# Kernel optimization log

Hardware: AMD Instinct MI355X
Metric: run time of the kernel (lower is better)

Reference implementation:

```python
import jax, jax.numpy as jnp
import numpy as np

NEG = -1e30  # stand-in for -inf on the H-attention diagonal (matches INF helper)


def _conv1x1(w, b, x):
    # w: [O, C], x: [B, C, H, W]
    return jnp.einsum('oc,bchw->bohw', w, x) + b[None, :, None, None]


def _cc_attn(q, k, v):
    """Criss-cross attention: q,k [B,Cq,H,W], v [B,C,H,W] -> [B,C,H,W]."""
    B, _, H, W = q.shape
    # column (H) energies: query at (h,w) attends to keys at (h', w)
    eH = jnp.einsum('bchw,bcjw->bhwj', q, k)  # [B,H,W,H]
    eye = jnp.eye(H, dtype=bool)[None, :, None, :]
    eH = jnp.where(eye, NEG, eH)  # mask h==h' (self counted once via W pass)
    # row (W) energies: query at (h,w) attends to keys at (h, w')
    eW = jnp.einsum('bchw,bchj->bhwj', q, k)  # [B,H,W,W]
    att = jax.nn.softmax(jnp.concatenate([eH, eW], axis=3), axis=3)  # [B,H,W,H+W]
    aH, aW = att[..., :H], att[..., H:]
    outH = jnp.einsum('bhwj,bcjw->bchw', aH, v)
    outW = jnp.einsum('bhwj,bchj->bchw', aW, v)
    return outH + outW


def setup_inputs() -> dict:
    key = jax.random.key(0)
    ks = jax.random.split(key, 14)
    B, C, H, W = 8, 256, 96, 96
    Cq = C // 8
    n = jax.random.normal
    return {
        'x': n(ks[0], (B, C, H, W), jnp.float32),
        'y': n(ks[1], (B, C, H, W), jnp.float32),
        'Wq': n(ks[2], (Cq, C), jnp.float32) * 0.05,
        'bq': n(ks[3], (Cq,), jnp.float32) * 0.05,
        'Wk': n(ks[4], (Cq, C), jnp.float32) * 0.05,
        'bk': n(ks[5], (Cq,), jnp.float32) * 0.05,
        'Wv': n(ks[6], (C, C), jnp.float32) * 0.05,
        'bv': n(ks[7], (C,), jnp.float32) * 0.05,
        'gamma1': n(ks[8], (1,), jnp.float32) * 0.1,
        'gamma2': n(ks[9], (1,), jnp.float32) * 0.1,
        'Wd': n(ks[10], (2 * C, 1, 3, 3), jnp.float32) * 0.1,  # depthwise, groups=2C
        'bd': n(ks[11], (2 * C,), jnp.float32) * 0.05,
        'Wp': n(ks[12], (C, 2 * C), jnp.float32) * 0.05,  # pointwise 1x1
        'bp': n(ks[13], (C,), jnp.float32) * 0.05,
    }


def reference(x, y, Wq, bq, Wk, bk, Wv, bv, gamma1, gamma2, Wd, bd, Wp, bp):
    qx = _conv1x1(Wq, bq, x)
    kx = _conv1x1(Wk, bk, x)
    vx = _conv1x1(Wv, bv, x)
    qy = _conv1x1(Wq, bq, y)
    ky = _conv1x1(Wk, bk, y)
    vy = _conv1x1(Wv, bv, y)
    # pass 1: attention weights from x, values from y
    out1 = gamma1[0] * _cc_attn(qx, kx, vy) + x
    # pass 2: attention weights from y, values from x
    out2 = gamma2[0] * _cc_attn(qy, ky, vx) + y
    z = jnp.concatenate([out1, out2], axis=1)  # [B, 2C, H, W]
    # depthwise 3x3 (groups = 2C), padding 1
    z = jax.lax.conv_general_dilated(
        z, Wd, window_strides=(1, 1), padding='SAME',
        feature_group_count=z.shape[1],
        dimension_numbers=('NCHW', 'OIHW', 'NCHW')) + bd[None, :, None, None]
    # pointwise 1x1 then LeakyReLU (torch default negative_slope=0.01)
    z = _conv1x1(Wp, bp, z)
    return jax.nn.leaky_relu(z, negative_slope=0.01)
```

## Files before the change

kernel.cpp:

```cpp
#include <hip/hip_runtime.h>
#include <hip/hip_bf16.h>

constexpr int kB  = 8;
constexpr int kC  = 256;
constexpr int kCq = 32;
constexpr int kH  = 96;
constexpr int kW  = 96;
constexpr int kP  = kH * kW;

using bf16x8 = __attribute__((ext_vector_type(8))) short;
using bf16x4 = __attribute__((ext_vector_type(4))) short;
using f32x4  = __attribute__((ext_vector_type(4))) float;

__device__ inline bf16x8 ld_lds8(const __hip_bfloat16* p) {
    bf16x4 lo = *(const bf16x4*)p;
    bf16x4 hi = *(const bf16x4*)(p + 4);
    return __builtin_shufflevector(lo, hi, 0, 1, 2, 3, 4, 5, 6, 7);
}

__global__ __launch_bounds__(256) void w_convert(
    const float* __restrict__ Wq, const float* __restrict__ Wk,
    const float* __restrict__ Wv,
    __hip_bfloat16* __restrict__ Wqkb, __hip_bfloat16* __restrict__ Wvb)
{
    const int i = blockIdx.x * 256 + threadIdx.x;
    if (i < 8192)       Wqkb[i] = __float2bfloat16(Wq[i]);
    else if (i < 16384) Wqkb[i] = __float2bfloat16(Wk[i - 8192]);
    else                Wvb[i - 16384] = __float2bfloat16(Wv[i - 16384]);
}

__global__ __launch_bounds__(256, 2) void qkv_mfma(
    const float* __restrict__ in_qk, const float* __restrict__ in_v,
    const __hip_bfloat16* __restrict__ Wqkb, const __hip_bfloat16* __restrict__ Wvb,
    const float* __restrict__ bq, const float* __restrict__ bk,
    const float* __restrict__ bv,
    __hip_bfloat16* __restrict__ Qbh, __hip_bfloat16* __restrict__ Qbl,
    __hip_bfloat16* __restrict__ Kbh, __hip_bfloat16* __restrict__ Kbl,
    __hip_bfloat16* __restrict__ Vpm, __hip_bfloat16* __restrict__ Vhw)
{
    __shared__ __align__(16) char smem[34816];
    __hip_bfloat16* sqb = (__hip_bfloat16*)smem;
    __hip_bfloat16* svb = sqb + 2 * 64 * 36;
    __hip_bfloat16* vt  = (__hip_bfloat16*)smem;

    const int b = blockIdx.y, t = threadIdx.x;
    const int wv = t >> 6, l = t & 63;
    const int n = l & 15, q = l >> 4;
    const int p0 = blockIdx.x * 64;
    const int p  = p0 + wv * 16 + n;
    const size_t bP = (size_t)b * kP;

    const float* __restrict__ xq = in_qk + (size_t)b * kC * kP + p0;
    const float* __restrict__ xv = in_v  + (size_t)b * kC * kP + p0;

    const int sc = t >> 4;
    const int sp = (t & 15) * 4;

    f32x4 acc[20];
#pragma unroll
    for (int i = 0; i < 20; i++) acc[i] = (f32x4)0.f;

    {
        float4 q0 = *(const float4*)&xq[(size_t)sc * kP + sp];
        float4 q1 = *(const float4*)&xq[(size_t)(16 + sc) * kP + sp];
        float4 v0 = *(const float4*)&xv[(size_t)sc * kP + sp];
        float4 v1 = *(const float4*)&xv[(size_t)(16 + sc) * kP + sp];
        float fq0[4] = { q0.x, q0.y, q0.z, q0.w };
        float fq1[4] = { q1.x, q1.y, q1.z, q1.w };
        float fv0[4] = { v0.x, v0.y, v0.z, v0.w };
        float fv1[4] = { v1.x, v1.y, v1.z, v1.w };
#pragma unroll
        for (int j = 0; j < 4; j++) {
            sqb[(sp + j) * 36 + sc]      = __float2bfloat16(fq0[j]);
            sqb[(sp + j) * 36 + 16 + sc] = __float2bfloat16(fq1[j]);
            svb[(sp + j) * 36 + sc]      = __float2bfloat16(fv0[j]);
            svb[(sp + j) * 36 + 16 + sc] = __float2bfloat16(fv1[j]);
        }
    }
    __syncthreads();

    int cur = 0;
    for (int kc = 0; kc < 8; kc++) {
        float4 nq0, nq1, nv0, nv1;
        if (kc < 7) {
            const size_t cb = (size_t)(kc + 1) * 32;
            nq0 = *(const float4*)&xq[(cb + sc) * kP + sp];
            nq1 = *(const float4*)&xq[(cb + 16 + sc) * kP + sp];
            nv0 = *(const float4*)&xv[(cb + sc) * kP + sp];
            nv1 = *(const float4*)&xv[(cb + 16 + sc) * kP + sp];
        }

        const int c0 = kc * 32 + q * 8;

        bf16x8 wq[4], wv2[16];
#pragma unroll
        for (int mt = 0; mt < 4; mt++)
            wq[mt] = *(const bf16x8*)(Wqkb + ((mt * 16 + n) << 8) + c0);
#pragma unroll
        for (int mt = 0; mt < 16; mt++)
            wv2[mt] = *(const bf16x8*)(Wvb + ((mt * 16 + n) << 8) + c0);

        const __hip_bfloat16* sqp = sqb + cur * 2304 + (wv * 16 + n) * 36 + q * 8;
        const __hip_bfloat16* svp = svb + cur * 2304 + (wv * 16 + n) * 36 + q * 8;
        bf16x8 bfq = ld_lds8(sqp);
        bf16x8 bfv = ld_lds8(svp);

#pragma unroll
        for (int mt = 0; mt < 4; mt++)
            acc[mt] = __builtin_amdgcn_mfma_f32_16x16x32_bf16(wq[mt], bfq, acc[mt], 0, 0, 0);
#pragma unroll
        for (int mt = 0; mt < 16; mt++)
            acc[4 + mt] = __builtin_amdgcn_mfma_f32_16x16x32_bf16(wv2[mt], bfv, acc[4 + mt], 0, 0, 0);

        if (kc < 7) {
            const int nb = cur ^ 1;
            __hip_bfloat16* dq = sqb + nb * 2304;
            __hip_bfloat16* dv = svb + nb * 2304;
            float fq0[4] = { nq0.x, nq0.y, nq0.z, nq0.w };
            float fq1[4] = { nq1.x, nq1.y, nq1.z, nq1.w };
            float fv0[4] = { nv0.x, nv0.y, nv0.z, nv0.w };
            float fv1[4] = { nv1.x, nv1.y, nv1.z, nv1.w };
#pragma unroll
            for (int j = 0; j < 4; j++) {
                dq[(sp + j) * 36 + sc]      = __float2bfloat16(fq0[j]);
                dq[(sp + j) * 36 + 16 + sc] = __float2bfloat16(fq1[j]);
                dv[(sp + j) * 36 + sc]      = __float2bfloat16(fv0[j]);
                dv[(sp + j) * 36 + 16 + sc] = __float2bfloat16(fv1[j]);
            }
        }
        __syncthreads();
        cur ^= 1;
    }

#pragma unroll
    for (int mt = 0; mt < 2; mt++) {
        float4 bias = *(const float4*)&bq[mt * 16 + q * 4];
        float vv[4] = { acc[mt][0] + bias.x, acc[mt][1] + bias.y,
                        acc[mt][2] + bias.z, acc[mt][3] + bias.w };
        union { ushort4 u; __hip_bfloat16 h[4]; } hi, lo;
#pragma unroll
        for (int r = 0; r < 4; r++) {
            __hip_bfloat16 h = __float2bfloat16(vv[r]);
            hi.h[r] = h;
            lo.h[r] = __float2bfloat16(vv[r] - __bfloat162float(h));
        }
        *(ushort4*)&Qbh[(bP + p) * kCq + mt * 16 + q * 4] = hi.u;
        *(ushort4*)&Qbl[(bP + p) * kCq + mt * 16 + q * 4] = lo.u;
    }
#pragma unroll
    for (int mt = 2; mt < 4; mt++) {
        float4 bias = *(const float4*)&bk[(mt - 2) * 16 + q * 4];
        float vv[4] = { acc[mt][0] + bias.x, acc[mt][1] + bias.y,
                        acc[mt][2] + bias.z, acc[mt][3] + bias.w };
        union { ushort4 u; __hip_bfloat16 h[4]; } hi, lo;
#pragma unroll
        for (int r = 0; r < 4; r++) {
            __hip_bfloat16 h = __float2bfloat16(vv[r]);
            hi.h[r] = h;
            lo.h[r] = __float2bfloat16(vv[r] - __bfloat162float(h));
        }
        *(ushort4*)&Kbh[(bP + p) * kCq + (mt - 2) * 16 + q * 4] = hi.u;
        *(ushort4*)&Kbl[(bP + p) * kCq + (mt - 2) * 16 + q * 4] = lo.u;
    }

#pragma unroll
    for (int mt = 0; mt < 16; mt++) {
        float4 bias = *(const float4*)&bv[mt * 16 + q * 4];
        float vv[4] = { acc[4 + mt][0] + bias.x, acc[4 + mt][1] + bias.y,
                        acc[4 + mt][2] + bias.z, acc[4 + mt][3] + bias.w };
        union { ushort4 u; __hip_bfloat16 h[4]; } pm;
#pragma unroll
        for (int r = 0; r < 4; r++) pm.h[r] = __float2bfloat16(vv[r]);
        *(ushort4*)&Vpm[(bP + p) * kC + mt * 16 + q * 4] = pm.u;
#pragma unroll
        for (int r = 0; r < 4; r++)
            vt[(mt * 16 + q * 4 + r) * 68 + wv * 16 + n] = pm.h[r];
    }
    __syncthreads();

    {
        __hip_bfloat16* dst = Vhw + ((size_t)b * kC + t) * kP + p0;
#pragma unroll
        for (int j = 0; j < 8; j++) {
            bf16x8 row = ld_lds8(&vt[t * 68 + j * 8]);
            *(bf16x8*)&dst[j * 8] = row;
        }
    }
}

__global__ __launch_bounds__(256) void cc_stats(
    const __hip_bfloat16* __restrict__ Qbh, const __hip_bfloat16* __restrict__ Qbl,
    const __hip_bfloat16* __restrict__ Kbh, const __hip_bfloat16* __restrict__ Kbl,
    float* __restrict__ Sm, float* __restrict__ Si)
{
    __shared__ __align__(16) __hip_bfloat16 QH[96][36], QLo[96][36];
    __shared__ __align__(16) __hip_bfloat16 KH[96][36], KLo[96][36];
    __shared__ __align__(16) float EL[96][97];
    const int w = blockIdx.x, b = blockIdx.y;
    const int t = threadIdx.x;
    const size_t bP = (size_t)b * kP;

    for (int idx = t; idx < 768; idx += 256) {
        int row = idx >> 3, ch = (idx & 7) * 4;
        size_t g = (bP + (size_t)row * kW + w) * kCq + ch;
        *(ushort4*)&QH[row][ch]  = *(const ushort4*)&Qbh[g];
        *(ushort4*)&QLo[row][ch] = *(const ushort4*)&Qbl[g];
        *(ushort4*)&KH[row][ch]  = *(const ushort4*)&Kbh[g];
        *(ushort4*)&KLo[row][ch] = *(const ushort4*)&Kbl[g];
    }
    __syncthreads();

    const int wv = t >> 6, l = t & 63, ln = l & 15, lq = l >> 4;
#pragma unroll
    for (int s = 0; s < 9; s++) {
        int tile = wv * 9 + s, it = tile / 6, jt = tile % 6;
        bf16x8 ah = ld_lds8(&QH[it * 16 + ln][lq * 8]);
        bf16x8 al = ld_lds8(&QLo[it * 16 + ln][lq * 8]);
        bf16x8 bh = ld_lds8(&KH[jt * 16 + ln][lq * 8]);
        bf16x8 bl = ld_lds8(&KLo[jt * 16 + ln][lq * 8]);
        f32x4 d = (f32x4)0.f;
        d = __builtin_amdgcn_mfma_f32_16x16x32_bf16(al, bh, d, 0, 0, 0);
        d = __builtin_amdgcn_mfma_f32_16x16x32_bf16(ah, bl, d, 0, 0, 0);
        d = __builtin_amdgcn_mfma_f32_16x16x32_bf16(ah, bh, d, 0, 0, 0);
#pragma unroll
        for (int r = 0; r < 4; r++)
            EL[it * 16 + lq * 4 + r][jt * 16 + ln] = d[r];
    }
    __syncthreads();

    const int sub = t & 7;
    for (int pi = t >> 3; pi < 96; pi += 32) {
        float ev[12];
        float mx = -3.0e38f;
#pragma unroll
        for (int k = 0; k < 12; k++) {
            int j = sub + 8 * k;
            float e = EL[pi][j];
            if (j == pi) e = -3.0e38f;
            ev[k] = e;
            mx = fmaxf(mx, e);
        }
#pragma unroll
        for (int k = 1; k < 8; k <<= 1) mx = fmaxf(mx, __shfl_xor(mx, k, 8));
        float ss = 0.f;
#pragma unroll
        for (int k = 0; k < 12; k++) ss += __expf(ev[k] - mx);
#pragma unroll
        for (int k = 1; k < 8; k <<= 1) ss += __shfl_xor(ss, k, 8);
        if (sub == 0) {
            Sm[bP + (size_t)pi * kW + w] = mx;
            Si[bP + (size_t)pi * kW + w] = ss;
        }
    }
}

__global__ __launch_bounds__(256) void cc_pass1(
    const __hip_bfloat16* __restrict__ Qbh, const __hip_bfloat16* __restrict__ Qbl,
    const __hip_bfloat16* __restrict__ Kbh, const __hip_bfloat16* __restrict__ Kbl,
    const __hip_bfloat16* __restrict__ Vhw,
    const float* __restrict__ res_in, const float* __restrict__ gamma_p,
    __hip_bfloat16* __restrict__ Zb, float* __restrict__ Sm, float* __restrict__ Si,
    int s_off)
{
    __shared__ __align__(16) __hip_bfloat16 QH[32][36], QLo[32][36];
    __shared__ __align__(16) __hip_bfloat16 KH[96][36], KLo[96][36];
    __shared__ __align__(16) float EL[32][97];
    __shared__ __align__(16) __hip_bfloat16 attL[32][100];
    __shared__ __align__(16) float rs[32][260];
    const int wt = blockIdx.x, h = blockIdx.y, b = blockIdx.z;
    const int w0 = wt * 32;
    const int t = threadIdx.x;
    const size_t bP = (size_t)b * kP;

    {
        int row = t >> 3, ch = (t & 7) * 4;
        size_t g = (bP + (size_t)h * kW + w0 + row) * kCq + ch;
        *(ushort4*)&QH[row][ch]  = *(const ushort4*)&Qbh[g];
        *(ushort4*)&QLo[row][ch] = *(const ushort4*)&Qbl[g];
    }
    for (int idx = t; idx < 768; idx += 256) {
        int row = idx >> 3, ch = (idx & 7) * 4;
        size_t g = (bP + (size_t)h * kW + row) * kCq + ch;
        *(ushort4*)&KH[row][ch]  = *(const ushort4*)&Kbh[g];
        *(ushort4*)&KLo[row][ch] = *(const ushort4*)&Kbl[g];
    }
    const float* __restrict__ res = res_in + (size_t)b * kC * kP + (size_t)h * kW + w0;
    {
        const int f4 = t & 7;
        int c2 = t >> 3;
#pragma unroll
        for (int it2 = 0; it2 < 8; it2++, c2 += 32) {
            float4 v = *(const float4*)&res[(size_t)c2 * kP + f4 * 4];
            rs[f4 * 4 + 0][c2] = v.x;
            rs[f4 * 4 + 1][c2] = v.y;
            rs[f4 * 4 + 2][c2] = v.z;
            rs[f4 * 4 + 3][c2] = v.w;
        }
    }
    __syncthreads();

    const int wv = t >> 6, l = t & 63, ln = l & 15, lq = l >> 4;
#pragma unroll
    for (int s = 0; s < 3; s++) {
        int tile = wv * 3 + s, it = tile / 6, jt = tile % 6;
        bf16x8 ah = ld_lds8(&QH[it * 16 + ln][lq * 8]);
        bf16x8 al = ld_lds8(&QLo[it * 16 + ln][lq * 8]);
        bf16x8 bh = ld_lds8(&KH[jt * 16 + ln][lq * 8]);
        bf16x8 bl = ld_lds8(&KLo[jt * 16 + ln][lq * 8]);
        f32x4 d = (f32x4)0.f;
        d = __builtin_amdgcn_mfma_f32_16x16x32_bf16(al, bh, d, 0, 0, 0);
        d = __builtin_amdgcn_mfma_f32_16x16x32_bf16(ah, bl, d, 0, 0, 0);
        d = __builtin_amdgcn_mfma_f32_16x16x32_bf16(ah, bh, d, 0, 0, 0);
#pragma unroll
        for (int r = 0; r < 4; r++)
            EL[it * 16 + lq * 4 + r][jt * 16 + ln] = d[r];
    }
    __syncthreads();

    {
        const int pi = t >> 3, sub = t & 7;
        size_t sidx = bP + (size_t)h * kW + w0 + pi;
        float mH = Sm[sidx], sH = Si[sidx];
        float ev[12];
        float mx = mH;
#pragma unroll
        for (int k = 0; k < 12; k++) {
            float e = EL[pi][sub + 8 * k];
            ev[k] = e;
            mx = fmaxf(mx, e);
        }
#pragma unroll
        for (int k = 1; k < 8; k <<= 1) mx = fmaxf(mx, __shfl_xor(mx, k, 8));
        float ss = 0.f;
#pragma unroll
        for (int k = 0; k < 12; k++) { float e = __expf(ev[k] - mx); ev[k] = e; ss += e; }
#pragma unroll
        for (int k = 1; k < 8; k <<= 1) ss += __shfl_xor(ss, k, 8);
        float stot = ss + sH * __expf(mH - mx);
        float inv = 1.0f / stot;
        if (sub == 0) { Sm[sidx] = mx; Si[sidx] = inv; }
#pragma unroll
        for (int k = 0; k < 12; k++)
            attL[pi][sub + 8 * k] = __float2bfloat16(ev[k] * inv);
    }
    __syncthreads();

    bf16x8 aF[2][3];
#pragma unroll
    for (int it = 0; it < 2; it++)
#pragma unroll
        for (int j3 = 0; j3 < 3; j3++)
            aF[it][j3] = ld_lds8(&attL[it * 16 + ln][j3 * 32 + lq * 8]);

    f32x4 acc[2][4];
#pragma unroll
    for (int it = 0; it < 2; it++)
#pragma unroll
        for (int c4 = 0; c4 < 4; c4++) acc[it][c4] = (f32x4)0.f;

#pragma unroll
    for (int c4 = 0; c4 < 4; c4++) {
        const int c = (wv * 4 + c4) * 16 + ln;
        const __hip_bfloat16* vr = Vhw + ((size_t)b * kC + c) * kP + (size_t)h * kW;
        bf16x8 bF0 = *(const bf16x8*)&vr[lq * 8];
        bf16x8 bF1 = *(const bf16x8*)&vr[32 + lq * 8];
        bf16x8 bF2 = *(const bf16x8*)&vr[64 + lq * 8];
#pragma unroll
        for (int it = 0; it < 2; it++) {
            acc[it][c4] = __builtin_amdgcn_mfma_f32_16x16x32_bf16(aF[it][0], bF0, acc[it][c4], 0, 0, 0);
            acc[it][c4] = __builtin_amdgcn_mfma_f32_16x16x32_bf16(aF[it][1], bF1, acc[it][c4], 0, 0, 0);
            acc[it][c4] = __builtin_amdgcn_mfma_f32_16x16x32_bf16(aF[it][2], bF2, acc[it][c4], 0, 0, 0);
        }
    }

    const float gamma = gamma_p[0];
#pragma unroll
    for (int c4 = 0; c4 < 4; c4++) {
        const int c = (wv * 4 + c4) * 16 + ln;
#pragma unroll
        for (int it = 0; it < 2; it++) {
#pragma unroll
            for (int r = 0; r < 4; r++) {
                int i = it * 16 + lq * 4 + r;
                float z = gamma * acc[it][c4][r] + rs[i][c];
                Zb[(bP + (size_t)h * kW + w0 + i) * 512 + s_off + c] = __float2bfloat16(z);
            }
        }
    }
}

__global__ __launch_bounds__(256) void cc_pass2(
    const __hip_bfloat16* __restrict__ Qbh, const __hip_bfloat16* __restrict__ Qbl,
    const __hip_bfloat16* __restrict__ Kbh, const __hip_bfloat16* __restrict__ Kbl,
    const __hip_bfloat16* __restrict__ Vpm,
    const float* __restrict__ gamma_p, __hip_bfloat16* __restrict__ Zb,
    const float* __restrict__ Sm, const float* __restrict__ Si, int s_off)
{
    __shared__ __align__(16) __hip_bfloat16 QH[32][36], QLo[32][36];
    __shared__ __align__(16) __hip_bfloat16 KH[96][36], KLo[96][36];
    __shared__ __align__(16) __hip_bfloat16 VL[96][260];
    __shared__ __align__(16) __hip_bfloat16 attL[32][100];
    const int ht = blockIdx.x, w = blockIdx.y, b = blockIdx.z;
    const int h0 = ht * 32;
    const int t = threadIdx.x;
    const size_t bP = (size_t)b * kP;

    {
        int row = t >> 3, ch = (t & 7) * 4;
        size_t g = (bP + (size_t)(h0 + row) * kW + w) * kCq + ch;
        *(ushort4*)&QH[row][ch]  = *(const ushort4*)&Qbh[g];
        *(ushort4*)&QLo[row][ch] = *(const ushort4*)&Qbl[g];
    }
    for (int idx = t; idx < 768; idx += 256) {
        int row = idx >> 3, ch = (idx & 7) * 4;
        size_t g = (bP + (size_t)row * kW + w) * kCq + ch;
        *(ushort4*)&KH[row][ch]  = *(const ushort4*)&Kbh[g];
        *(ushort4*)&KLo[row][ch] = *(const ushort4*)&Kbl[g];
    }
    for (int idx = t; idx < 96 * 32; idx += 256) {
        int j = idx >> 5, cg = (idx & 31) * 8;
        const ushort4* src = (const ushort4*)&Vpm[(bP + (size_t)j * kW + w) * kC + cg];
        ushort4 v0 = src[0], v1 = src[1];
        *(ushort4*)&VL[j][cg]     = v0;
        *(ushort4*)&VL[j][cg + 4] = v1;
    }
    __syncthreads();

    const int wv = t >> 6, l = t & 63, ln = l & 15, lq = l >> 4;
#pragma unroll
    for (int s = 0; s < 3; s++) {
        int tile = wv * 3 + s, it = tile / 6, jt = tile % 6;
        bf16x8 ah = ld_lds8(&QH[it * 16 + ln][lq * 8]);
        bf16x8 al = ld_lds8(&QLo[it * 16 + ln][lq * 8]);
        bf16x8 bh = ld_lds8(&KH[jt * 16 + ln][lq * 8]);
        bf16x8 bl = ld_lds8(&KLo[jt * 16 + ln][lq * 8]);
        f32x4 d = (f32x4)0.f;
        d = __builtin_amdgcn_mfma_f32_16x16x32_bf16(al, bh, d, 0, 0, 0);
        d = __builtin_amdgcn_mfma_f32_16x16x32_bf16(ah, bl, d, 0, 0, 0);
        d = __builtin_amdgcn_mfma_f32_16x16x32_bf16(ah, bh, d, 0, 0, 0);
        const int j = jt * 16 + ln;
#pragma unroll
        for (int r = 0; r < 4; r++) {
            int i = it * 16 + lq * 4 + r;
            size_t sidx = bP + (size_t)(h0 + i) * kW + w;
            float m = Sm[sidx], inv = Si[sidx];
            float a = (j == h0 + i) ? 0.f : __expf(d[r] - m) * inv;
            attL[i][j] = __float2bfloat16(a);
        }
    }
    __syncthreads();

    bf16x8 aF[2][3];
#pragma unroll
    for (int it = 0; it < 2; it++)
#pragma unroll
        for (int j3 = 0; j3 < 3; j3++)
            aF[it][j3] = ld_lds8(&attL[it * 16 + ln][j3 * 32 + lq * 8]);

    f32x4 acc[2][4];
#pragma unroll
    for (int it = 0; it < 2; it++)
#pragma unroll
        for (int c4 = 0; c4 < 4; c4++) acc[it][c4] = (f32x4)0.f;

#pragma unroll
    for (int c4 = 0; c4 < 4; c4++) {
        const int c = (wv * 4 + c4) * 16 + ln;
#pragma unroll
        for (int j3 = 0; j3 < 3; j3++) {
            union { bf16x8 v; __hip_bfloat16 h[8]; } bF;
#pragma unroll
            for (int jj = 0; jj < 8; jj++)
                bF.h[jj] = VL[j3 * 32 + lq * 8 + jj][c];
#pragma unroll
            for (int it = 0; it < 2; it++)
                acc[it][c4] = __builtin_amdgcn_mfma_f32_16x16x32_bf16(aF[it][j3], bF.v, acc[it][c4], 0, 0, 0);
        }
    }

    const float gamma = gamma_p[0];
#pragma unroll
    for (int c4 = 0; c4 < 4; c4++) {
        const int c = (wv * 4 + c4) * 16 + ln;
#pragma unroll
        for (int it = 0; it < 2; it++) {
#pragma unroll
            for (int r = 0; r < 4; r++) {
                int i = it * 16 + lq * 4 + r;
                size_t zi = (bP + (size_t)(h0 + i) * kW + w) * 512 + s_off + c;
                float old = __bfloat162float(Zb[zi]);
                Zb[zi] = __float2bfloat16(old + gamma * acc[it][c4][r]);
            }
        }
    }
}

__global__ __launch_bounds__(256) void wp_convert(
    const float* __restrict__ Wp, __hip_bfloat16* __restrict__ Wpb)
{
    const int i = blockIdx.x * 256 + threadIdx.x;
    Wpb[i] = __float2bfloat16(Wp[i]);
}

__global__ __launch_bounds__(256, 6) void dwpw(
    const __hip_bfloat16* __restrict__ Zb,
    const float* __restrict__ Wdw, const float* __restrict__ bd,
    const __hip_bfloat16* __restrict__ Wpb, const float* __restrict__ bp,
    float* __restrict__ out)
{
    __shared__ __align__(16) __hip_bfloat16 zs[16][520];

    const int wt = blockIdx.x, h = blockIdx.y, b = blockIdx.z;
    const int w0 = wt * 16;
    const int t = threadIdx.x;
    const size_t bP = (size_t)b * kP;

    const int l = t & 63, wv = t >> 6;
    const int lo16 = l & 15, q = l >> 4;

    {
        const float b0 = bd[2 * t], b1 = bd[2 * t + 1];
        const uint* __restrict__ Zp = (const uint*)Zb + bP * 256 + t;
        const float* __restrict__ wdp0 = Wdw + (size_t)(2 * t) * 9;
        const float* __restrict__ wdp1 = Wdw + (size_t)(2 * t + 1) * 9;

#pragma unroll
        for (int j0 = 0; j0 < 16; j0 += 8) {
            float a0[8], a1[8];
#pragma unroll
            for (int j = 0; j < 8; j++) { a0[j] = b0; a1[j] = b1; }

#pragma unroll
            for (int r = 0; r < 3; r++) {
                const int hh = h + r - 1;
                const int hcl = hh < 0 ? 0 : (hh > kH - 1 ? kH - 1 : hh);
                const bool hv = (hh >= 0) && (hh < kH);

                uint raw[10];
#pragma unroll
                for (int col = 0; col < 10; col++) {
                    const int ww = w0 + j0 - 1 + col;
                    const int wcl = ww < 0 ? 0 : (ww > kW - 1 ? kW - 1 : ww);
                    const bool v = hv && (ww >= 0) && (ww < kW);
                    uint val = Zp[(size_t)(hcl * kW + wcl) * 256];
                    raw[col] = v ? val : 0u;
                }
                float w0r[3], w1r[3];
#pragma unroll
                for (int dw = 0; dw < 3; dw++) {
                    w0r[dw] = wdp0[r * 3 + dw];
                    w1r[dw] = wdp1[r * 3 + dw];
                }
                float2 f[10];
#pragma unroll
                for (int col = 0; col < 10; col++) {
                    __hip_bfloat162 z2 = *(const __hip_bfloat162*)&raw[col];
                    f[col] = __bfloat1622float2(z2);
                }
#pragma unroll
                for (int j = 0; j < 8; j++) {
#pragma unroll
                    for (int dw = 0; dw < 3; dw++) {
                        a0[j] += w0r[dw] * f[j + dw].x;
                        a1[j] += w1r[dw] * f[j + dw].y;
                    }
                }
            }

#pragma unroll
            for (int j = 0; j < 8; j++) {
                __hip_bfloat162 pz;
                pz.x = __float2bfloat16(a0[j]);
                pz.y = __float2bfloat16(a1[j]);
                ((__hip_bfloat162*)&zs[j0 + j][0])[t] = pz;
            }
        }
    }
    __syncthreads();

    const bf16x8* __restrict__ Bb[4];
#pragma unroll
    for (int nt = 0; nt < 4; nt++)
        Bb[nt] = (const bf16x8*)(Wpb + (size_t)(wv * 64 + nt * 16 + lo16) * 512);

    f32x4 acc[4];
#pragma unroll
    for (int nt = 0; nt < 4; nt++) acc[nt] = (f32x4)0.f;

    for (int kc = 0; kc < 16; kc++) {
        bf16x8 a0 = ld_lds8(&zs[lo16][kc * 32 + q * 8]);
#pragma unroll
        for (int nt = 0; nt < 4; nt++) {
            bf16x8 w = Bb[nt][kc * 4 + q];
            acc[nt] = __builtin_amdgcn_mfma_f32_16x16x32_bf16(a0, w, acc[nt], 0, 0, 0);
        }
    }

#pragma unroll
    for (int nt = 0; nt < 4; nt++) {
        const int ol = wv * 64 + nt * 16 + lo16;
        const float bias = bp[ol];
        float4 rv;
        float v0 = acc[nt][0] + bias; rv.x = v0 > 0.f ? v0 : 0.01f * v0;
        float v1 = acc[nt][1] + bias; rv.y = v1 > 0.f ? v1 : 0.01f * v1;
        float v2 = acc[nt][2] + bias; rv.z = v2 > 0.f ? v2 : 0.01f * v2;
        float v3 = acc[nt][3] + bias; rv.w = v3 > 0.f ? v3 : 0.01f * v3;
        *(float4*)&out[((size_t)b * 256 + ol) * kP + (size_t)h * kW + w0 + q * 4] = rv;
    }
}

extern "C" void kernel_launch(void* const* d_in, const int* in_sizes, int n_in,
                              void* d_out, int out_size, void* d_ws, size_t ws_size,
                              hipStream_t stream)
{
    const float* x   = (const float*)d_in[0];
    const float* y   = (const float*)d_in[1];
    const float* Wq  = (const float*)d_in[2];
    const float* bq  = (const float*)d_in[3];
    const float* Wk  = (const float*)d_in[4];
    const float* bk  = (const float*)d_in[5];
    const float* Wv  = (const float*)d_in[6];
    const float* bv  = (const float*)d_in[7];
    const float* g1  = (const float*)d_in[8];
    const float* g2  = (const float*)d_in[9];
    const float* Wdw = (const float*)d_in[10];
    const float* bd  = (const float*)d_in[11];
    const float* Wp  = (const float*)d_in[12];
    const float* bp  = (const float*)d_in[13];
    float* out = (float*)d_out;

    char* wsb = (char*)d_ws;
    __hip_bfloat16* Zb  = (__hip_bfloat16*)wsb;
    __hip_bfloat16* Qbh = (__hip_bfloat16*)(wsb + 75497472);
    __hip_bfloat16* Qbl = Qbh + 2359296;
    __hip_bfloat16* Kbh = (__hip_bfloat16*)(wsb + 84934656);
    __hip_bfloat16* Kbl = Kbh + 2359296;
    float* Sm = (float*)(wsb + 94371840);
    float* Si = (float*)(wsb + 94666752);
    __hip_bfloat16* Wqkb = (__hip_bfloat16*)Sm;
    __hip_bfloat16* Wvb  = ((__hip_bfloat16*)Sm) + 16384;
    __hip_bfloat16* Wpb  = (__hip_bfloat16*)(wsb + 75497472);
    __hip_bfloat16* Vpm  = (__hip_bfloat16*)d_out;
    __hip_bfloat16* Vhw  = Vpm + 18874368;

    hipLaunchKernelGGL(w_convert, dim3(320), dim3(256), 0, stream,
                       Wq, Wk, Wv, Wqkb, Wvb);
    hipLaunchKernelGGL(qkv_mfma, dim3(kP / 64, kB), dim3(256), 0, stream,
                       x, y, Wqkb, Wvb, bq, bk, bv, Qbh, Qbl, Kbh, Kbl, Vpm, Vhw);
    hipLaunchKernelGGL(cc_stats, dim3(kW, kB), dim3(256), 0, stream,
                       Qbh, Qbl, Kbh, Kbl, Sm, Si);
    hipLaunchKernelGGL(cc_pass1, dim3(kW / 32, kH, kB), dim3(256), 0, stream,
                       Qbh, Qbl, Kbh, Kbl, Vhw, x, g1, Zb, Sm, Si, 0);
    hipLaunchKernelGGL(cc_pass2, dim3(kH / 32, kW, kB), dim3(256), 0, stream,
                       Qbh, Qbl, Kbh, Kbl, Vpm, g1, Zb, Sm, Si, 0);
    hipLaunchKernelGGL(w_convert, dim3(320), dim3(256), 0, stream,
                       Wq, Wk, Wv, Wqkb, Wvb);
    hipLaunchKernelGGL(qkv_mfma, dim3(kP / 64, kB), dim3(256), 0, stream,
                       y, x, Wqkb, Wvb, bq, bk, bv, Qbh, Qbl, Kbh, Kbl, Vpm, Vhw);
    hipLaunchKernelGGL(cc_stats, dim3(kW, kB), dim3(256), 0, stream,
                       Qbh, Qbl, Kbh, Kbl, Sm, Si);
    hipLaunchKernelGGL(cc_pass1, dim3(kW / 32, kH, kB), dim3(256), 0, stream,
                       Qbh, Qbl, Kbh, Kbl, Vhw, y, g2, Zb, Sm, Si, 256);
    hipLaunchKernelGGL(cc_pass2, dim3(kH / 32, kW, kB), dim3(256), 0, stream,
                       Qbh, Qbl, Kbh, Kbl, Vpm, g2, Zb, Sm, Si, 256);
    hipLaunchKernelGGL(wp_convert, dim3(512), dim3(256), 0, stream, Wp, Wpb);
    hipLaunchKernelGGL(dwpw, dim3(kW / 16, kH, kB), dim3(256), 0, stream,
                       Zb, Wdw, bd, Wpb, bp, out);
}
```

Measured before the change: 834.9 us.

## Stage depthwise conv input window in LDS via async global-to-LDS copies

The dwpw kernel now loads the full 3x18-pixel by 512-channel bf16 window into shared memory with global_load_lds 16-byte async copies. The depthwise 3x3 then reads from LDS and computes all 16 output columns in one pass, instead of issuing two overlapping 10-column gathers from global memory. This cuts redundant global loads and replaces 4-byte strided reads with 16-byte coalesced ones. In exchange, LDS use grows to about 70KB and the occupancy hint drops from 6 to 2 blocks, which may reduce latency hiding in the pointwise MFMA phase.

```diff
diff --git a/kernel.cpp b/kernel.cpp
--- a/kernel.cpp
+++ b/kernel.cpp
@@ -16,6 +16,12 @@
     bf16x4 lo = *(const bf16x4*)p;
     bf16x4 hi = *(const bf16x4*)(p + 4);
     return __builtin_shufflevector(lo, hi, 0, 1, 2, 3, 4, 5, 6, 7);
+}
+
+__device__ inline void async_copy16(const void* g, void* l) {
+    __builtin_amdgcn_global_load_lds(
+        (const __attribute__((address_space(1))) unsigned int*)g,
+        (__attribute__((address_space(3))) unsigned int*)l, 16, 0, 0);
 }
 
 __global__ __launch_bounds__(256) void w_convert(
@@ -502,13 +508,15 @@
     Wpb[i] = __float2bfloat16(Wp[i]);
 }
 
-__global__ __launch_bounds__(256, 6) void dwpw(
+__global__ __launch_bounds__(256, 2) void dwpw(
     const __hip_bfloat16* __restrict__ Zb,
     const float* __restrict__ Wdw, const float* __restrict__ bd,
     const __hip_bfloat16* __restrict__ Wpb, const float* __restrict__ bp,
     float* __restrict__ out)
 {
-    __shared__ __align__(16) __hip_bfloat16 zs[16][520];
+    __shared__ __align__(16) char smem[71936];
+    __hip_bfloat16* win = (__hip_bfloat16*)smem;
+    __hip_bfloat16 (*zs)[520] = (__hip_bfloat16 (*)[520])(smem + 55296);
 
     const int wt = blockIdx.x, h = blockIdx.y, b = blockIdx.z;
     const int w0 = wt * 16;
@@ -519,61 +527,63 @@
     const int lo16 = l & 15, q = l >> 4;
 
     {
+        const char* zbase = (const char*)(Zb + bP * 512);
+        for (int s = wv; s < 54; s += 4) {
+            const int r = s / 18, col = s - r * 18;
+            int hh = h + r - 1;
+            const int hcl = hh < 0 ? 0 : (hh > kH - 1 ? kH - 1 : hh);
+            int wwx = w0 - 1 + col;
+            const int wcl = wwx < 0 ? 0 : (wwx > kW - 1 ? kW - 1 : wwx);
+            const int px = hcl * kW + wcl;
+            async_copy16(zbase + (size_t)px * 1024 + (size_t)l * 16,
+                         (char*)win + (size_t)s * 1024);
+        }
+    }
+    __syncthreads();
+
+    {
+        float wd0[9], wd1[9];
+#pragma unroll
+        for (int k = 0; k < 9; k++) {
+            wd0[k] = Wdw[(size_t)(2 * t) * 9 + k];
+            wd1[k] = Wdw[(size_t)(2 * t + 1) * 9 + k];
+        }
         const float b0 = bd[2 * t], b1 = bd[2 * t + 1];
-        const uint* __restrict__ Zp = (const uint*)Zb + bP * 256 + t;
-        const float* __restrict__ wdp0 = Wdw + (size_t)(2 * t) * 9;
-        const float* __restrict__ wdp1 = Wdw + (size_t)(2 * t + 1) * 9;
-
-#pragma unroll
-        for (int j0 = 0; j0 < 16; j0 += 8) {
-            float a0[8], a1[8];
-#pragma unroll
-            for (int j = 0; j < 8; j++) { a0[j] = b0; a1[j] = b1; }
-
-#pragma unroll
-            for (int r = 0; r < 3; r++) {
-                const int hh = h + r - 1;
-                const int hcl = hh < 0 ? 0 : (hh > kH - 1 ? kH - 1 : hh);
-                const bool hv = (hh >= 0) && (hh < kH);
-
-                uint raw[10];
-#pragma unroll
-                for (int col = 0; col < 10; col++) {
-                    const int ww = w0 + j0 - 1 + col;
-                    const int wcl = ww < 0 ? 0 : (ww > kW - 1 ? kW - 1 : ww);
-                    const bool v = hv && (ww >= 0) && (ww < kW);
-                    uint val = Zp[(size_t)(hcl * kW + wcl) * 256];
-                    raw[col] = v ? val : 0u;
-                }
-                float w0r[3], w1r[3];
+        const uint* __restrict__ winU = (const uint*)win;
+
+        float a0[16], a1[16];
+#pragma unroll
+        for (int j = 0; j < 16; j++) { a0[j] = b0; a1[j] = b1; }
+
+#pragma unroll
+        for (int r = 0; r < 3; r++) {
+            const int hh = h + r - 1;
+            const bool hv = (hh >= 0) && (hh < kH);
+#pragma unroll
+            for (int col = 0; col < 18; col++) {
+                const int wwx = w0 - 1 + col;
+                const bool v = hv && (wwx >= 0) && (wwx < kW);
+                uint raw = winU[(r * 18 + col) * 256 + t];
+                raw = v ? raw : 0u;
+                __hip_bfloat162 z2 = *(const __hip_bfloat162*)&raw;
+                float2 f = __bfloat1622float2(z2);
 #pragma unroll
                 for (int dw = 0; dw < 3; dw++) {
-                    w0r[dw] = wdp0[r * 3 + dw];
-                    w1r[dw] = wdp1[r * 3 + dw];
-                }
-                float2 f[10];
-#pragma unroll
-                for (int col = 0; col < 10; col++) {
-                    __hip_bfloat162 z2 = *(const __hip_bfloat162*)&raw[col];
-                    f[col] = __bfloat1622float2(z2);
-                }
-#pragma unroll
-                for (int j = 0; j < 8; j++) {
-#pragma unroll
-                    for (int dw = 0; dw < 3; dw++) {
-                        a0[j] += w0r[dw] * f[j + dw].x;
-                        a1[j] += w1r[dw] * f[j + dw].y;
+                    const int j = col - dw;
+                    if (j >= 0 && j < 16) {
+                        a0[j] += wd0[r * 3 + dw] * f.x;
+                        a1[j] += wd1[r * 3 + dw] * f.y;
                     }
                 }
             }
-
-#pragma unroll
-            for (int j = 0; j < 8; j++) {
-                __hip_bfloat162 pz;
-                pz.x = __float2bfloat16(a0[j]);
-                pz.y = __float2bfloat16(a1[j]);
-                ((__hip_bfloat162*)&zs[j0 + j][0])[t] = pz;
-            }
+        }
+
+#pragma unroll
+        for (int j = 0; j < 16; j++) {
+            __hip_bfloat162 pz;
+            pz.x = __float2bfloat16(a0[j]);
+            pz.y = __float2bfloat16(a1[j]);
+            ((__hip_bfloat162*)&zs[j][0])[t] = pz;
         }
     }
     __syncthreads();
```

Result: no change. 832.2 us (-0.3%).

## Restructure depthwise stage to vectorized 8-channel loads with LDS-staged transposed weights

Applied to the files above, without the earlier changes.

The depthwise 3x3 part of the fused depthwise+pointwise kernel now gives each thread one pixel and eight contiguous channels. Each thread issues 16-byte loads per tap instead of 4-byte strided loads across ten columns per row. A small kernel transposes the depthwise weights to a tap-major layout, and each block stages them into shared memory so they can be read as float4. This adds 18KB of LDS per block and lowers the occupancy hint from 6 to 4, trading occupancy for wider, more coalesced memory access.

```diff
diff --git a/kernel.cpp b/kernel.cpp
--- a/kernel.cpp
+++ b/kernel.cpp
@@ -502,12 +502,23 @@
     Wpb[i] = __float2bfloat16(Wp[i]);
 }
 
-__global__ __launch_bounds__(256, 6) void dwpw(
+__global__ __launch_bounds__(256) void wdw_convert(
+    const float* __restrict__ Wdw, float* __restrict__ Wdwt)
+{
+    const int i = blockIdx.x * 256 + threadIdx.x;
+    if (i < 9 * 512) {
+        const int k = i / 512, c = i - k * 512;
+        Wdwt[i] = Wdw[(size_t)c * 9 + k];
+    }
+}
+
+__global__ __launch_bounds__(256, 4) void dwpw(
     const __hip_bfloat16* __restrict__ Zb,
-    const float* __restrict__ Wdw, const float* __restrict__ bd,
+    const float* __restrict__ Wdwt, const float* __restrict__ bd,
     const __hip_bfloat16* __restrict__ Wpb, const float* __restrict__ bp,
     float* __restrict__ out)
 {
+    __shared__ __align__(16) float wdl[9][512];
     __shared__ __align__(16) __hip_bfloat16 zs[16][520];
 
     const int wt = blockIdx.x, h = blockIdx.y, b = blockIdx.z;
@@ -518,62 +529,61 @@
     const int l = t & 63, wv = t >> 6;
     const int lo16 = l & 15, q = l >> 4;
 
+    for (int i = t; i < 9 * 512; i += 256)
+        ((float*)wdl)[i] = Wdwt[i];
+    __syncthreads();
+
     {
-        const float b0 = bd[2 * t], b1 = bd[2 * t + 1];
-        const uint* __restrict__ Zp = (const uint*)Zb + bP * 256 + t;
-        const float* __restrict__ wdp0 = Wdw + (size_t)(2 * t) * 9;
-        const float* __restrict__ wdp1 = Wdw + (size_t)(2 * t + 1) * 9;
-
-#pragma unroll
-        for (int j0 = 0; j0 < 16; j0 += 8) {
-            float a0[8], a1[8];
-#pragma unroll
-            for (int j = 0; j < 8; j++) { a0[j] = b0; a1[j] = b1; }
-
+        const int px = t & 15, choct = t >> 4;
+        const bool rvm = (h > 0), rvp = (h < kH - 1);
+        const __hip_bfloat16* __restrict__ Zrow = Zb + bP * 512;
+
+        for (int cg = 0; cg < 4; cg++) {
+            const int ch0 = (cg * 16 + choct) * 8;
+
+            bf16x8 raw[9];
+            bool val[9];
 #pragma unroll
             for (int r = 0; r < 3; r++) {
                 const int hh = h + r - 1;
                 const int hcl = hh < 0 ? 0 : (hh > kH - 1 ? kH - 1 : hh);
-                const bool hv = (hh >= 0) && (hh < kH);
-
-                uint raw[10];
-#pragma unroll
-                for (int col = 0; col < 10; col++) {
-                    const int ww = w0 + j0 - 1 + col;
+                const bool hv = (r == 1) || (r == 0 ? rvm : rvp);
+#pragma unroll
+                for (int dw = 0; dw < 3; dw++) {
+                    const int ww = w0 + px + dw - 1;
                     const int wcl = ww < 0 ? 0 : (ww > kW - 1 ? kW - 1 : ww);
-                    const bool v = hv && (ww >= 0) && (ww < kW);
-                    uint val = Zp[(size_t)(hcl * kW + wcl) * 256];
-                    raw[col] = v ? val : 0u;
-                }
-                float w0r[3], w1r[3];
-#pragma unroll
-                for (int dw = 0; dw < 3; dw++) {
-                    w0r[dw] = wdp0[r * 3 + dw];
-                    w1r[dw] = wdp1[r * 3 + dw];
-                }
-                float2 f[10];
-#pragma unroll
-                for (int col = 0; col < 10; col++) {
-                    __hip_bfloat162 z2 = *(const __hip_bfloat162*)&raw[col];
-                    f[col] = __bfloat1622float2(z2);
-                }
-#pragma unroll
-                for (int j = 0; j < 8; j++) {
-#pragma unroll
-                    for (int dw = 0; dw < 3; dw++) {
-                        a0[j] += w0r[dw] * f[j + dw].x;
-                        a1[j] += w1r[dw] * f[j + dw].y;
-                    }
+                    raw[r * 3 + dw] =
+                        *(const bf16x8*)&Zrow[(size_t)(hcl * kW + wcl) * 512 + ch0];
+                    val[r * 3 + dw] = hv && (ww >= 0) && (ww < kW);
                 }
             }
 
-#pragma unroll
-            for (int j = 0; j < 8; j++) {
-                __hip_bfloat162 pz;
-                pz.x = __float2bfloat16(a0[j]);
-                pz.y = __float2bfloat16(a1[j]);
-                ((__hip_bfloat162*)&zs[j0 + j][0])[t] = pz;
+            float4 bA = *(const float4*)&bd[ch0];
+            float4 bB = *(const float4*)&bd[ch0 + 4];
+            float a[8] = { bA.x, bA.y, bA.z, bA.w, bB.x, bB.y, bB.z, bB.w };
+
+#pragma unroll
+            for (int k = 0; k < 9; k++) {
+                union { bf16x8 v; __hip_bfloat162 h2[4]; } u;
+                u.v = raw[k];
+                float4 wA = *(const float4*)&wdl[k][ch0];
+                float4 wB = *(const float4*)&wdl[k][ch0 + 4];
+                float wk[8] = { wA.x, wA.y, wA.z, wA.w, wB.x, wB.y, wB.z, wB.w };
+                const bool v = val[k];
+#pragma unroll
+                for (int jj = 0; jj < 4; jj++) {
+                    float2 f = __bfloat1622float2(u.h2[jj]);
+                    f.x = v ? f.x : 0.f;
+                    f.y = v ? f.y : 0.f;
+                    a[2 * jj]     += wk[2 * jj]     * f.x;
+                    a[2 * jj + 1] += wk[2 * jj + 1] * f.y;
+                }
             }
+
+            union { bf16x8 v; __hip_bfloat16 h8[8]; } o;
+#pragma unroll
+            for (int j = 0; j < 8; j++) o.h8[j] = __float2bfloat16(a[j]);
+            *(bf16x8*)&zs[px][ch0] = o.v;
         }
     }
     __syncthreads();
@@ -640,6 +650,7 @@
     __hip_bfloat16* Wqkb = (__hip_bfloat16*)Sm;
     __hip_bfloat16* Wvb  = ((__hip_bfloat16*)Sm) + 16384;
     __hip_bfloat16* Wpb  = (__hip_bfloat16*)(wsb + 75497472);
+    float* Wdwt = (float*)(wsb + 84934656);
     __hip_bfloat16* Vpm  = (__hip_bfloat16*)d_out;
     __hip_bfloat16* Vhw  = Vpm + 18874368;
 
@@ -664,6 +675,7 @@
     hipLaunchKernelGGL(cc_pass2, dim3(kH / 32, kW, kB), dim3(256), 0, stream,
                        Qbh, Qbl, Kbh, Kbl, Vpm, g2, Zb, Sm, Si, 256);
     hipLaunchKernelGGL(wp_convert, dim3(512), dim3(256), 0, stream, Wp, Wpb);
+    hipLaunchKernelGGL(wdw_convert, dim3(18), dim3(256), 0, stream, Wdw, Wdwt);
     hipLaunchKernelGGL(dwpw, dim3(kW / 16, kH, kB), dim3(256), 0, stream,
-                       Zb, Wdw, bd, Wpb, bp, out);
-}
+                       Zb, Wdwt, bd, Wpb, bp, out);
+}
```

Result: slower. 886.8 us (+6.2%).
